# Optimization experiments

Hardware: AMD Instinct MI355X
Metric: run time of the kernel (lower is better)

## Reference

```python
import jax, jax.numpy as jnp
import numpy as np

N_NODES = 100000
N_EDGES = 1600000
N_GRAPHS = 128
BEHAVIOR_DIM = 32
LLM_DIM = 768
LLM_PROJ = 32
HIDDEN = 64
NUM_CLASSES = 2
INPUT_DIM = 64 + 16 + LLM_PROJ + BEHAVIOR_DIM  # 144


def gcn_conv(h, edge_index, edge_weight, W, b, n):
    """PyG GCNConv: linear -> gcn_norm with self-loops -> scatter-add at target."""
    h = h @ W  # [N, out]
    row, col = edge_index[0], edge_index[1]
    loop = jnp.arange(n)
    row_f = jnp.concatenate([row, loop])
    col_f = jnp.concatenate([col, loop])
    ew_f = jnp.concatenate([edge_weight, jnp.ones((n,), h.dtype)])
    deg = jax.ops.segment_sum(ew_f, col_f, num_segments=n)
    dinv = jnp.where(deg > 0, jax.lax.rsqrt(deg), 0.0)
    norm = dinv[row_f] * ew_f * dinv[col_f]  # [E+N]
    out = jax.ops.segment_sum(norm[:, None] * h[row_f], col_f, num_segments=n)
    return out + b


def global_mean_pool(x, batch, num_graphs):
    s = jax.ops.segment_sum(x, batch, num_segments=num_graphs)
    cnt = jax.ops.segment_sum(jnp.ones((x.shape[0],), x.dtype), batch, num_segments=num_graphs)
    return s / jnp.maximum(cnt, 1.0)[:, None]


def setup_inputs() -> dict:
    key = jax.random.key(0)
    ks = jax.random.split(key, 16)
    inp = {
        "x_names": jax.random.randint(ks[0], (N_NODES,), 0, 20000),
        "x_types": jax.random.randint(ks[1], (N_NODES,), 0, 100),
        "x_behaviors": jax.random.normal(ks[2], (N_NODES, BEHAVIOR_DIM), jnp.float32),
        "edge_index": jax.random.randint(ks[3], (2, N_EDGES), 0, N_NODES),
        "edge_weight": jax.random.uniform(ks[4], (N_EDGES,), jnp.float32),
        "batch": jnp.sort(jax.random.randint(ks[5], (N_NODES,), 0, N_GRAPHS)),
        "llm_features": jax.random.normal(ks[6], (N_NODES, LLM_DIM), jnp.float32),
        # parameters
        "name_emb": jax.random.normal(ks[7], (20000, 64), jnp.float32),
        "type_emb": jax.random.normal(ks[8], (100, 16), jnp.float32),
        "llm_proj_w": jax.random.normal(ks[9], (LLM_DIM, LLM_PROJ), jnp.float32) * 0.02,
        "llm_proj_b": jnp.zeros((LLM_PROJ,), jnp.float32),
        "conv1_w": jax.random.normal(ks[10], (INPUT_DIM, HIDDEN), jnp.float32) * 0.08,
        "conv1_b": jnp.zeros((HIDDEN,), jnp.float32),
        "conv2_w": jax.random.normal(ks[11], (HIDDEN, HIDDEN), jnp.float32) * 0.12,
        "conv2_b": jnp.zeros((HIDDEN,), jnp.float32),
        "cls_w": jax.random.normal(ks[12], (HIDDEN, NUM_CLASSES), jnp.float32) * 0.12,
        "cls_b": jnp.zeros((NUM_CLASSES,), jnp.float32),
    }
    return inp


def reference(x_names, x_types, x_behaviors, edge_index, edge_weight, batch,
              llm_features, name_emb, type_emb, llm_proj_w, llm_proj_b,
              conv1_w, conv1_b, conv2_w, conv2_b, cls_w, cls_b):
    n = x_names.shape[0]
    name_feat = name_emb[x_names]          # [N, 64]
    type_feat = type_emb[x_types]          # [N, 16]
    llm_feat = llm_features @ llm_proj_w + llm_proj_b  # [N, 32]
    x = jnp.concatenate([name_feat, type_feat, llm_feat, x_behaviors], axis=1)
    # dropout is identity in eval mode
    x = jax.nn.relu(gcn_conv(x, edge_index, edge_weight, conv1_w, conv1_b, n))
    x = jax.nn.relu(gcn_conv(x, edge_index, edge_weight, conv2_w, conv2_b, n))
    x = global_mean_pool(x, batch, N_GRAPHS)  # [G, HIDDEN]
    return x @ cls_w + cls_b                   # [G, 2]
```

## Files before the change

kernel.cpp:

```cpp
#include <hip/hip_runtime.h>
#include <cstdint>
#include <cstddef>

typedef __attribute__((ext_vector_type(8))) short bf16x8;
typedef __attribute__((ext_vector_type(4))) float f32x4;


__device__ __forceinline__ unsigned bf_rne(float x) {
  unsigned u = __float_as_uint(x);
  return (u + 0x7FFFu + ((u >> 16) & 1u)) >> 16;
}

__device__ __forceinline__ void split1(float x, short& hi, short& lo) {
  unsigned hb = bf_rne(x);
  hi = (short)hb;
  float fh = __uint_as_float(hb << 16);
  lo = (short)bf_rne(x - fh);
}

__device__ __forceinline__ void split8(const float4& p, const float4& q, bf16x8& h, bf16x8& l) {
  short hh, ll;
  split1(p.x, hh, ll); h[0] = hh; l[0] = ll;
  split1(p.y, hh, ll); h[1] = hh; l[1] = ll;
  split1(p.z, hh, ll); h[2] = hh; l[2] = ll;
  split1(p.w, hh, ll); h[3] = hh; l[3] = ll;
  split1(q.x, hh, ll); h[4] = hh; l[4] = ll;
  split1(q.y, hh, ll); h[5] = hh; l[5] = ll;
  split1(q.z, hh, ll); h[6] = hh; l[6] = ll;
  split1(q.w, hh, ll); h[7] = hh; l[7] = ll;
}


__global__ void prep1_kernel(const float* __restrict__ pw, const float* __restrict__ pb,
                             const float* __restrict__ w1,
                             short* __restrict__ Bh, short* __restrict__ Bl,
                             float* __restrict__ biasf) {
  int idx = blockIdx.x * 256 + threadIdx.x;
  if (idx < 896 * 64) {
    int gk = idx >> 6, col = idx & 63;
    float val;
    if (gk < 768) {
      float acc = 0.0f;
      #pragma unroll 8
      for (int m = 0; m < 32; ++m) acc = fmaf(pw[gk * 32 + m], w1[(80 + m) * 64 + col], acc);
      val = acc;
    } else if (gk < 832) val = w1[(gk - 768) * 64 + col];
    else if (gk < 848)   val = w1[(64 + gk - 832) * 64 + col];
    else if (gk < 864)   val = w1[(112 + gk - 848) * 64 + col];
    else if (gk < 880)   val = w1[(128 + gk - 864) * 64 + col];
    else                 val = 0.0f;
    int chunk = gk >> 5, k = gk & 31;
    int g, j;
    if (k < 16) { g = k >> 2; j = k & 3; } else { int k2 = k - 16; g = k2 >> 2; j = 4 + (k2 & 3); }
    size_t o = ((size_t)(chunk * 4 + g) * 64 + col) * 8 + j;
    short hh, ll; split1(val, hh, ll);
    Bh[o] = hh; Bl[o] = ll;
  } else if (idx < 896 * 64 + 64) {
    int col = idx - 896 * 64;
    float acc = 0.0f;
    for (int m = 0; m < 32; ++m) acc = fmaf(pb[m], w1[(80 + m) * 64 + col], acc);
    biasf[col] = acc;
  }
}

__global__ void prep2_kernel(const float* __restrict__ w2,
                             short* __restrict__ B2h, short* __restrict__ B2l) {
  int idx = blockIdx.x * 256 + threadIdx.x;
  if (idx >= 64 * 64) return;
  int gk = idx >> 6, col = idx & 63;
  float val = w2[gk * 64 + col];
  int chunk = gk >> 5, k = gk & 31;
  int g, j;
  if (k < 16) { g = k >> 2; j = k & 3; } else { int k2 = k - 16; g = k2 >> 2; j = 4 + (k2 & 3); }
  size_t o = ((size_t)(chunk * 4 + g) * 64 + col) * 8 + j;
  short hh, ll; split1(val, hh, ll);
  B2h[o] = hh; B2l[o] = ll;
}


__global__ void cnt_kernel(const int* __restrict__ ei, int* __restrict__ cnt, int E) {
  int e = blockIdx.x * 256 + threadIdx.x;
  if (e < E) atomicAdd(&cnt[ei[E + e]], 1);
}

__global__ __launch_bounds__(256) void scan_blk(const int* __restrict__ cnt,
                                                int* __restrict__ colp,
                                                int* __restrict__ bsum, int n) {
  __shared__ int ws[4];
  int t = threadIdx.x, lane = t & 63, w = t >> 6;
  int i = blockIdx.x * 256 + t;
  int v = (i < n) ? cnt[i] : 0;
  int x = v;
  #pragma unroll
  for (int off = 1; off < 64; off <<= 1) { int y = __shfl_up(x, off); if (lane >= off) x += y; }
  if (lane == 63) ws[w] = x;
  __syncthreads();
  if (t == 0) {
    int s = 0;
    #pragma unroll
    for (int k = 0; k < 4; ++k) { int tmp = ws[k]; ws[k] = s; s += tmp; }
    bsum[blockIdx.x] = s;
  }
  __syncthreads();
  if (i < n) colp[i] = ws[w] + x - v;
}

__global__ __launch_bounds__(512) void scan_top(int* __restrict__ bsum,
                                                int* __restrict__ colp, int nb, int n) {
  __shared__ int ws[8];
  int t = threadIdx.x, lane = t & 63, w = t >> 6;
  int v = (t < nb) ? bsum[t] : 0;
  int x = v;
  #pragma unroll
  for (int off = 1; off < 64; off <<= 1) { int y = __shfl_up(x, off); if (lane >= off) x += y; }
  if (lane == 63) ws[w] = x;
  __syncthreads();
  if (t == 0) {
    int s = 0;
    #pragma unroll
    for (int k = 0; k < 8; ++k) { int tmp = ws[k]; ws[k] = s; s += tmp; }
  }
  __syncthreads();
  int excl = ws[w] + x - v;
  if (t < nb) bsum[t] = excl;
  if (t == nb - 1) colp[n] = excl + v;
}

__global__ void scan_add(int* __restrict__ colp, int* __restrict__ fillp,
                         const int* __restrict__ bsum, int n) {
  int i = blockIdx.x * 256 + threadIdx.x;
  if (i < n) {
    int c = colp[i] + bsum[blockIdx.x];
    colp[i] = c;
    fillp[i] = c;
  }
}

__global__ void fill_kernel(const int* __restrict__ ei, const float* __restrict__ ew,
                            int* __restrict__ fillp, int2* __restrict__ csr, int E) {
  int e = blockIdx.x * 256 + threadIdx.x;
  if (e >= E) return;
  int row = ei[e], col = ei[E + e];
  int pos = atomicAdd(&fillp[col], 1);
  csr[pos] = make_int2(row, __float_as_int(ew[e]));
}

__global__ void degsum_kernel(const int* __restrict__ colp, const int2* __restrict__ csr,
                              float* __restrict__ dinv, int n) {
  int j = blockIdx.x * 256 + threadIdx.x;
  if (j >= n) return;
  int e0 = colp[j], e1 = colp[j + 1];
  float s = 1.0f;
  for (int e = e0; e < e1; ++e) s += __int_as_float(csr[e].y);
  dinv[j] = rsqrtf(s);
}

__global__ void wfix_kernel(int2* __restrict__ csr, const float* __restrict__ dinv, int E) {
  int i = blockIdx.x * 256 + threadIdx.x;
  if (i >= E) return;
  int2 m = csr[i];
  csr[i] = make_int2(m.x, __float_as_int(__int_as_float(m.y) * dinv[m.x]));
}


__device__ __forceinline__ void mfma24(f32x4 (&acc)[2][4],
                                       const bf16x8& ah0, const bf16x8& al0,
                                       const bf16x8& ah1, const bf16x8& al1,
                                       const bf16x8 (&bh)[4], const bf16x8 (&bl)[4]) {
  #pragma unroll
  for (int ct = 0; ct < 4; ++ct) {
    acc[0][ct] = __builtin_amdgcn_mfma_f32_16x16x32_bf16(ah0, bh[ct], acc[0][ct], 0, 0, 0);
    acc[0][ct] = __builtin_amdgcn_mfma_f32_16x16x32_bf16(ah0, bl[ct], acc[0][ct], 0, 0, 0);
    acc[0][ct] = __builtin_amdgcn_mfma_f32_16x16x32_bf16(al0, bh[ct], acc[0][ct], 0, 0, 0);
  }
  #pragma unroll
  for (int ct = 0; ct < 4; ++ct) {
    acc[1][ct] = __builtin_amdgcn_mfma_f32_16x16x32_bf16(ah1, bh[ct], acc[1][ct], 0, 0, 0);
    acc[1][ct] = __builtin_amdgcn_mfma_f32_16x16x32_bf16(ah1, bl[ct], acc[1][ct], 0, 0, 0);
    acc[1][ct] = __builtin_amdgcn_mfma_f32_16x16x32_bf16(al1, bh[ct], acc[1][ct], 0, 0, 0);
  }
}

__device__ __forceinline__ void loadB(const short* __restrict__ Bh, const short* __restrict__ Bl,
                                      int c, int g, int r16, bf16x8 (&bh)[4], bf16x8 (&bl)[4]) {
  #pragma unroll
  for (int ct = 0; ct < 4; ++ct) {
    size_t o = ((size_t)(c * 4 + g) * 64 + ct * 16 + r16) * 8;
    bh[ct] = *(const bf16x8*)(Bh + o);
    bl[ct] = *(const bf16x8*)(Bl + o);
  }
}

__global__ __launch_bounds__(256, 3) void gemm1_kernel(
    const float* __restrict__ llm, const short* __restrict__ Bh, const short* __restrict__ Bl,
    const int* __restrict__ names, const int* __restrict__ types,
    const float* __restrict__ beh, const float* __restrict__ nemb,
    const float* __restrict__ temb, const float* __restrict__ biasf,
    float* __restrict__ out, int n)
{
  int nwg = gridDim.x;
  int b = blockIdx.x;
  int q = nwg >> 3, r = nwg & 7;
  int xcd = b & 7, idx = b >> 3;
  int swz = (xcd < r ? xcd * (q + 1) : r * (q + 1) + (xcd - r) * q) + idx;

  int w = swz * 4 + (threadIdx.x >> 6);
  int nw = (n + 31) >> 5;
  if (w >= nw) return;
  int lane = threadIdx.x & 63;
  int g = lane >> 4, r16 = lane & 15;
  int base = w * 32;

  int arow0 = base + r16;      if (arow0 > n - 1) arow0 = n - 1;
  int arow1 = base + 16 + r16; if (arow1 > n - 1) arow1 = n - 1;
  int nm0 = names[arow0], nm1 = names[arow1];
  int tp0 = types[arow0], tp1 = types[arow1];

  const float* pA0 = llm + (size_t)arow0 * 768 + g * 4;
  const float* pA1 = llm + (size_t)arow1 * 768 + g * 4;

  f32x4 acc[2][4];
  #pragma unroll
  for (int i = 0; i < 2; ++i)
    #pragma unroll
    for (int j = 0; j < 4; ++j) { acc[i][j][0] = 0.f; acc[i][j][1] = 0.f; acc[i][j][2] = 0.f; acc[i][j][3] = 0.f; }

  float4 X0l = *(const float4*)(pA0 +  0), X0h = *(const float4*)(pA0 + 16);
  float4 X1l = *(const float4*)(pA1 +  0), X1h = *(const float4*)(pA1 + 16);
  float4 Y0l = *(const float4*)(pA0 + 32), Y0h = *(const float4*)(pA0 + 48);
  float4 Y1l = *(const float4*)(pA1 + 32), Y1h = *(const float4*)(pA1 + 48);

  bf16x8 bh[4], bl[4], ah0, al0, ah1, al1;

  #pragma unroll 1
  for (int cc = 0; cc < 11; ++cc) {
    const int c = cc * 2;
    loadB(Bh, Bl, c, g, r16, bh, bl);
    split8(X0l, X0h, ah0, al0);
    split8(X1l, X1h, ah1, al1);
    X0l = *(const float4*)(pA0 + (c + 2) * 32);
    X0h = *(const float4*)(pA0 + (c + 2) * 32 + 16);
    X1l = *(const float4*)(pA1 + (c + 2) * 32);
    X1h = *(const float4*)(pA1 + (c + 2) * 32 + 16);
    mfma24(acc, ah0, al0, ah1, al1, bh, bl);
    loadB(Bh, Bl, c + 1, g, r16, bh, bl);
    split8(Y0l, Y0h, ah0, al0);
    split8(Y1l, Y1h, ah1, al1);
    Y0l = *(const float4*)(pA0 + (c + 3) * 32);
    Y0h = *(const float4*)(pA0 + (c + 3) * 32 + 16);
    Y1l = *(const float4*)(pA1 + (c + 3) * 32);
    Y1h = *(const float4*)(pA1 + (c + 3) * 32 + 16);
    mfma24(acc, ah0, al0, ah1, al1, bh, bl);
  }

  loadB(Bh, Bl, 22, g, r16, bh, bl);
  split8(X0l, X0h, ah0, al0);
  split8(X1l, X1h, ah1, al1);
  mfma24(acc, ah0, al0, ah1, al1, bh, bl);

  loadB(Bh, Bl, 23, g, r16, bh, bl);
  split8(Y0l, Y0h, ah0, al0);
  split8(Y1l, Y1h, ah1, al1);
  mfma24(acc, ah0, al0, ah1, al1, bh, bl);

  const float* pN0 = nemb + (size_t)nm0 * 64 + g * 4;
  const float* pN1 = nemb + (size_t)nm1 * 64 + g * 4;
  #pragma unroll
  for (int t = 0; t < 2; ++t) {
    float4 l0 = *(const float4*)(pN0 + t * 32), h0 = *(const float4*)(pN0 + t * 32 + 16);
    float4 l1 = *(const float4*)(pN1 + t * 32), h1 = *(const float4*)(pN1 + t * 32 + 16);
    loadB(Bh, Bl, 24 + t, g, r16, bh, bl);
    split8(l0, h0, ah0, al0);
    split8(l1, h1, ah1, al1);
    mfma24(acc, ah0, al0, ah1, al1, bh, bl);
  }
  {
    float4 l0 = *(const float4*)(temb + (size_t)tp0 * 16 + g * 4);
    float4 h0 = *(const float4*)(beh + (size_t)arow0 * 32 + g * 4);
    float4 l1 = *(const float4*)(temb + (size_t)tp1 * 16 + g * 4);
    float4 h1 = *(const float4*)(beh + (size_t)arow1 * 32 + g * 4);
    loadB(Bh, Bl, 26, g, r16, bh, bl);
    split8(l0, h0, ah0, al0);
    split8(l1, h1, ah1, al1);
    mfma24(acc, ah0, al0, ah1, al1, bh, bl);
  }
  {
    const float4 z = make_float4(0.f, 0.f, 0.f, 0.f);
    float4 l0 = *(const float4*)(beh + (size_t)arow0 * 32 + 16 + g * 4);
    float4 l1 = *(const float4*)(beh + (size_t)arow1 * 32 + 16 + g * 4);
    loadB(Bh, Bl, 27, g, r16, bh, bl);
    split8(l0, z, ah0, al0);
    split8(l1, z, ah1, al1);
    mfma24(acc, ah0, al0, ah1, al1, bh, bl);
  }

  #pragma unroll
  for (int ct = 0; ct < 4; ++ct) {
    int col = ct * 16 + r16;
    float bf = biasf[col];
    #pragma unroll
    for (int rr = 0; rr < 4; ++rr) {
      int node0 = base + g * 4 + rr;
      if (node0 < n) out[(size_t)node0 * 64 + col] = acc[0][ct][rr] + bf;
      int node1 = base + 16 + g * 4 + rr;
      if (node1 < n) out[(size_t)node1 * 64 + col] = acc[1][ct][rr] + bf;
    }
  }
}


__global__ __launch_bounds__(256, 4) void gemm2_kernel(
    const float* __restrict__ h, const short* __restrict__ B2h, const short* __restrict__ B2l,
    float* __restrict__ out, int n)
{
  int w = blockIdx.x * 4 + (threadIdx.x >> 6);
  int nw = (n + 31) >> 5;
  if (w >= nw) return;
  int lane = threadIdx.x & 63;
  int g = lane >> 4, r16 = lane & 15;
  int base = w * 32;
  int arow0 = base + r16;      if (arow0 > n - 1) arow0 = n - 1;
  int arow1 = base + 16 + r16; if (arow1 > n - 1) arow1 = n - 1;

  f32x4 acc[2][4];
  #pragma unroll
  for (int i = 0; i < 2; ++i)
    #pragma unroll
    for (int j = 0; j < 4; ++j) { acc[i][j][0] = 0.f; acc[i][j][1] = 0.f; acc[i][j][2] = 0.f; acc[i][j][3] = 0.f; }

  #pragma unroll
  for (int c = 0; c < 2; ++c) {
    bf16x8 bh[4], bl[4];
    loadB(B2h, B2l, c, g, r16, bh, bl);
    const float* p0 = h + (size_t)arow0 * 64 + c * 32 + g * 4;
    const float* p1 = h + (size_t)arow1 * 64 + c * 32 + g * 4;
    float4 lo0 = *(const float4*)p0, hi0 = *(const float4*)(p0 + 16);
    float4 lo1 = *(const float4*)p1, hi1 = *(const float4*)(p1 + 16);
    bf16x8 ah0, al0, ah1, al1;
    split8(lo0, hi0, ah0, al0);
    split8(lo1, hi1, ah1, al1);
    mfma24(acc, ah0, al0, ah1, al1, bh, bl);
  }

  #pragma unroll
  for (int ct = 0; ct < 4; ++ct) {
    int col = ct * 16 + r16;
    #pragma unroll
    for (int rr = 0; rr < 4; ++rr) {
      int node0 = base + g * 4 + rr;
      if (node0 < n) out[(size_t)node0 * 64 + col] = acc[0][ct][rr];
      int node1 = base + 16 + g * 4 + rr;
      if (node1 < n) out[(size_t)node1 * 64 + col] = acc[1][ct][rr];
    }
  }
}


__global__ __launch_bounds__(256) void agg_kernel(
    const float* __restrict__ h, const int* __restrict__ colp,
    const int2* __restrict__ csr, const float* __restrict__ dinv,
    const float* __restrict__ bias, float* __restrict__ out, int n)
{
  int wid = threadIdx.x >> 6, lane = threadIdx.x & 63;
  int j = blockIdx.x * 4 + wid;
  if (j >= n) return;
  float dj = dinv[j];
  float hj = h[(size_t)j * 64 + lane];
  int e0 = colp[j], e1 = colp[j + 1];
  float s = 0.0f;
  int e = e0;
  for (; e + 4 <= e1; e += 4) {
    int2 m0 = csr[e], m1 = csr[e + 1], m2 = csr[e + 2], m3 = csr[e + 3];
    float f0 = h[(size_t)m0.x * 64 + lane];
    float f1 = h[(size_t)m1.x * 64 + lane];
    float f2 = h[(size_t)m2.x * 64 + lane];
    float f3 = h[(size_t)m3.x * 64 + lane];
    s = fmaf(__int_as_float(m0.y), f0, s);
    s = fmaf(__int_as_float(m1.y), f1, s);
    s = fmaf(__int_as_float(m2.y), f2, s);
    s = fmaf(__int_as_float(m3.y), f3, s);
  }
  for (; e < e1; ++e) {
    int2 m = csr[e];
    s = fmaf(__int_as_float(m.y), h[(size_t)m.x * 64 + lane], s);
  }
  float acc = bias[lane] + dj * fmaf(dj, hj, s);
  out[(size_t)j * 64 + lane] = fmaxf(acc, 0.0f);
}


__global__ __launch_bounds__(256) void pool_kernel(const float* __restrict__ x,
                                                   const int* __restrict__ batch,
                                                   float* __restrict__ pooled, int n) {
  __shared__ float red[4][64];
  __shared__ int range_s[2];
  int gph = blockIdx.x;
  int tid = threadIdx.x, wid = tid >> 6, lane = tid & 63;
  if (tid < 2) {
    int target = gph + tid;
    int lo = 0, hi = n;
    while (lo < hi) { int m = (lo + hi) >> 1; if (batch[m] < target) lo = m + 1; else hi = m; }
    range_s[tid] = lo;
  }
  __syncthreads();
  int lo = range_s[0], hi = range_s[1];
  float acc = 0.0f;
  for (int i = lo + wid; i < hi; i += 4) acc += x[(size_t)i * 64 + lane];
  red[wid][lane] = acc;
  __syncthreads();
  if (tid < 64) {
    float sum = red[0][lane] + red[1][lane] + red[2][lane] + red[3][lane];
    float cntf = (float)(hi - lo);
    pooled[gph * 64 + lane] = sum / fmaxf(cntf, 1.0f);
  }
}

__global__ void cls_kernel(const float* __restrict__ pooled, const float* __restrict__ cw,
                           const float* __restrict__ cb, float* __restrict__ out) {
  int t = threadIdx.x;
  int gph = t >> 1, c = t & 1;
  float acc = cb[c];
  #pragma unroll 8
  for (int k = 0; k < 64; ++k) acc = fmaf(pooled[gph * 64 + k], cw[k * 2 + c], acc);
  out[gph * 2 + c] = acc;
}


extern "C" void kernel_launch(void* const* d_in, const int* in_sizes, int n_in,
                              void* d_out, int out_size, void* d_ws, size_t ws_size,
                              hipStream_t stream) {
  const int*   x_names  = (const int*)  d_in[0];
  const int*   x_types  = (const int*)  d_in[1];
  const float* behav    = (const float*)d_in[2];
  const int*   ei       = (const int*)  d_in[3];
  const float* ew       = (const float*)d_in[4];
  const int*   batch    = (const int*)  d_in[5];
  const float* llm      = (const float*)d_in[6];
  const float* name_emb = (const float*)d_in[7];
  const float* type_emb = (const float*)d_in[8];
  const float* pw       = (const float*)d_in[9];
  const float* pb       = (const float*)d_in[10];
  const float* w1       = (const float*)d_in[11];
  const float* b1       = (const float*)d_in[12];
  const float* w2       = (const float*)d_in[13];
  const float* b2       = (const float*)d_in[14];
  const float* cw       = (const float*)d_in[15];
  const float* cb       = (const float*)d_in[16];

  const int N = in_sizes[0];
  const int E = in_sizes[4];
  const int nb = (N + 255) / 256;
  const int eb = (E + 255) / 256;
  const int nwaves = (N + 31) / 32;
  const int gblocks = (nwaves + 3) / 4;

  char* p = (char*)d_ws;
  auto alloc = [&](size_t bytes) -> void* {
    void* r = (void*)p; p += (bytes + 255) & ~(size_t)255; return r;
  };
  float* dinv   = (float*)alloc((size_t)N * 4);
  int*   cnt    = (int*)  alloc((size_t)N * 4);
  int*   colp   = (int*)  alloc((size_t)(N + 1) * 4);
  int*   fillp  = (int*)  alloc((size_t)N * 4);
  int2*  csr    = (int2*) alloc((size_t)E * 8);
  int*   bsum   = (int*)  alloc((size_t)(nb + 1) * 4);
  short* Bh     = (short*)alloc((size_t)896 * 64 * 2);
  short* Bl     = (short*)alloc((size_t)896 * 64 * 2);
  short* B2h    = (short*)alloc((size_t)64 * 64 * 2);
  short* B2l    = (short*)alloc((size_t)64 * 64 * 2);
  float* biasf  = (float*)alloc((size_t)64 * 4);
  float* bufX   = (float*)alloc((size_t)N * 64 * 4);
  float* bufY   = (float*)alloc((size_t)N * 64 * 4);
  float* pooled = (float*)alloc((size_t)128 * 64 * 4);
  (void)ws_size; (void)n_in; (void)out_size;

  prep1_kernel<<<(896 * 64 + 64 + 255) / 256, 256, 0, stream>>>(pw, pb, w1, Bh, Bl, biasf);
  prep2_kernel<<<16, 256, 0, stream>>>(w2, B2h, B2l);
  hipMemsetAsync(cnt, 0, (size_t)N * 4, stream);
  cnt_kernel<<<eb, 256, 0, stream>>>(ei, cnt, E);
  scan_blk<<<nb, 256, 0, stream>>>(cnt, colp, bsum, N);
  scan_top<<<1, 512, 0, stream>>>(bsum, colp, nb, N);
  scan_add<<<nb, 256, 0, stream>>>(colp, fillp, bsum, N);
  fill_kernel<<<eb, 256, 0, stream>>>(ei, ew, fillp, csr, E);
  degsum_kernel<<<nb, 256, 0, stream>>>(colp, csr, dinv, N);
  wfix_kernel<<<eb, 256, 0, stream>>>(csr, dinv, E);

  gemm1_kernel<<<gblocks, 256, 0, stream>>>(llm, Bh, Bl, x_names, x_types, behav,
                                            name_emb, type_emb, biasf, bufX, N);
  agg_kernel<<<(N + 3) / 4, 256, 0, stream>>>(bufX, colp, csr, dinv, b1, bufY, N);
  gemm2_kernel<<<gblocks, 256, 0, stream>>>(bufY, B2h, B2l, bufX, N);
  agg_kernel<<<(N + 3) / 4, 256, 0, stream>>>(bufX, colp, csr, dinv, b2, bufY, N);
  pool_kernel<<<128, 256, 0, stream>>>(bufY, batch, pooled, N);
  cls_kernel<<<1, 256, 0, stream>>>(pooled, cw, cb, (float*)d_out);
}
```

Baseline: 548.2 us.

## Use single fp16 MFMA for GEMM1, fold source-degree scaling into GEMM epilogues

GEMM1 drops the three-pass bf16 hi/lo split emulation and runs one fp16 MFMA pass over fp16 weights, with a three-stage register prefetch and sched barriers. The per-edge wfix pass is removed: the GEMM epilogues now multiply each output row by dinv, so aggregation uses raw edge weights. The aggregation loop is unrolled to 8 with two accumulators, and the two prep kernels are merged. The fp16 path cuts MFMA work and prologue traffic, but it loses accuracy and could overflow on large inputs.

New measurement: 497.2 us. -9.3%, faster.

```diff
diff --git a/kernel.cpp b/kernel.cpp
--- a/kernel.cpp
+++ b/kernel.cpp
@@ -3,6 +3,7 @@
 #include <cstddef>
 
 typedef __attribute__((ext_vector_type(8))) short bf16x8;
+typedef __attribute__((ext_vector_type(8))) _Float16 f16x8;
 typedef __attribute__((ext_vector_type(4))) float f32x4;
 
 
@@ -30,11 +31,18 @@
   split1(q.w, hh, ll); h[7] = hh; l[7] = ll;
 }
 
-
-__global__ void prep1_kernel(const float* __restrict__ pw, const float* __restrict__ pb,
-                             const float* __restrict__ w1,
-                             short* __restrict__ Bh, short* __restrict__ Bl,
-                             float* __restrict__ biasf) {
+__device__ __forceinline__ f16x8 cvt8(const float4& p, const float4& q) {
+  f16x8 r;
+  r[0] = (_Float16)p.x; r[1] = (_Float16)p.y; r[2] = (_Float16)p.z; r[3] = (_Float16)p.w;
+  r[4] = (_Float16)q.x; r[5] = (_Float16)q.y; r[6] = (_Float16)q.z; r[7] = (_Float16)q.w;
+  return r;
+}
+
+
+__global__ void prep_kernel(const float* __restrict__ pw, const float* __restrict__ pb,
+                            const float* __restrict__ w1, const float* __restrict__ w2,
+                            _Float16* __restrict__ Bf, float* __restrict__ biasf,
+                            short* __restrict__ B2h, short* __restrict__ B2l) {
   int idx = blockIdx.x * 256 + threadIdx.x;
   if (idx < 896 * 64) {
     int gk = idx >> 6, col = idx & 63;
@@ -52,29 +60,23 @@
     int chunk = gk >> 5, k = gk & 31;
     int g, j;
     if (k < 16) { g = k >> 2; j = k & 3; } else { int k2 = k - 16; g = k2 >> 2; j = 4 + (k2 & 3); }
-    size_t o = ((size_t)(chunk * 4 + g) * 64 + col) * 8 + j;
-    short hh, ll; split1(val, hh, ll);
-    Bh[o] = hh; Bl[o] = ll;
+    Bf[((size_t)(chunk * 4 + g) * 64 + col) * 8 + j] = (_Float16)val;
   } else if (idx < 896 * 64 + 64) {
     int col = idx - 896 * 64;
     float acc = 0.0f;
     for (int m = 0; m < 32; ++m) acc = fmaf(pb[m], w1[(80 + m) * 64 + col], acc);
     biasf[col] = acc;
-  }
-}
-
-__global__ void prep2_kernel(const float* __restrict__ w2,
-                             short* __restrict__ B2h, short* __restrict__ B2l) {
-  int idx = blockIdx.x * 256 + threadIdx.x;
-  if (idx >= 64 * 64) return;
-  int gk = idx >> 6, col = idx & 63;
-  float val = w2[gk * 64 + col];
-  int chunk = gk >> 5, k = gk & 31;
-  int g, j;
-  if (k < 16) { g = k >> 2; j = k & 3; } else { int k2 = k - 16; g = k2 >> 2; j = 4 + (k2 & 3); }
-  size_t o = ((size_t)(chunk * 4 + g) * 64 + col) * 8 + j;
-  short hh, ll; split1(val, hh, ll);
-  B2h[o] = hh; B2l[o] = ll;
+  } else if (idx < 896 * 64 + 64 + 64 * 64) {
+    int q2 = idx - (896 * 64 + 64);
+    int gk = q2 >> 6, col = q2 & 63;
+    float val = w2[gk * 64 + col];
+    int chunk = gk >> 5, k = gk & 31;
+    int g, j;
+    if (k < 16) { g = k >> 2; j = k & 3; } else { int k2 = k - 16; g = k2 >> 2; j = 4 + (k2 & 3); }
+    size_t o = ((size_t)(chunk * 4 + g) * 64 + col) * 8 + j;
+    short hh, ll; split1(val, hh, ll);
+    B2h[o] = hh; B2l[o] = ll;
+  }
 }
 
 
@@ -155,54 +157,35 @@
   dinv[j] = rsqrtf(s);
 }
 
-__global__ void wfix_kernel(int2* __restrict__ csr, const float* __restrict__ dinv, int E) {
-  int i = blockIdx.x * 256 + threadIdx.x;
-  if (i >= E) return;
-  int2 m = csr[i];
-  csr[i] = make_int2(m.x, __float_as_int(__int_as_float(m.y) * dinv[m.x]));
-}
-
-
-__device__ __forceinline__ void mfma24(f32x4 (&acc)[2][4],
-                                       const bf16x8& ah0, const bf16x8& al0,
-                                       const bf16x8& ah1, const bf16x8& al1,
-                                       const bf16x8 (&bh)[4], const bf16x8 (&bl)[4]) {
+
+__device__ __forceinline__ void loadBf(const _Float16* __restrict__ Bf, int c, int g, int r16,
+                                       f16x8 (&bf)[4]) {
+  #pragma unroll
+  for (int ct = 0; ct < 4; ++ct)
+    bf[ct] = *(const f16x8*)(Bf + ((size_t)(c * 4 + g) * 64 + ct * 16 + r16) * 8);
+}
+
+__device__ __forceinline__ void mfma8(f32x4 (&acc)[2][4], const f16x8& a0, const f16x8& a1,
+                                      const f16x8 (&bf)[4]) {
   #pragma unroll
   for (int ct = 0; ct < 4; ++ct) {
-    acc[0][ct] = __builtin_amdgcn_mfma_f32_16x16x32_bf16(ah0, bh[ct], acc[0][ct], 0, 0, 0);
-    acc[0][ct] = __builtin_amdgcn_mfma_f32_16x16x32_bf16(ah0, bl[ct], acc[0][ct], 0, 0, 0);
-    acc[0][ct] = __builtin_amdgcn_mfma_f32_16x16x32_bf16(al0, bh[ct], acc[0][ct], 0, 0, 0);
-  }
-  #pragma unroll
-  for (int ct = 0; ct < 4; ++ct) {
-    acc[1][ct] = __builtin_amdgcn_mfma_f32_16x16x32_bf16(ah1, bh[ct], acc[1][ct], 0, 0, 0);
-    acc[1][ct] = __builtin_amdgcn_mfma_f32_16x16x32_bf16(ah1, bl[ct], acc[1][ct], 0, 0, 0);
-    acc[1][ct] = __builtin_amdgcn_mfma_f32_16x16x32_bf16(al1, bh[ct], acc[1][ct], 0, 0, 0);
-  }
-}
-
-__device__ __forceinline__ void loadB(const short* __restrict__ Bh, const short* __restrict__ Bl,
-                                      int c, int g, int r16, bf16x8 (&bh)[4], bf16x8 (&bl)[4]) {
-  #pragma unroll
-  for (int ct = 0; ct < 4; ++ct) {
-    size_t o = ((size_t)(c * 4 + g) * 64 + ct * 16 + r16) * 8;
-    bh[ct] = *(const bf16x8*)(Bh + o);
-    bl[ct] = *(const bf16x8*)(Bl + o);
+    acc[0][ct] = __builtin_amdgcn_mfma_f32_16x16x32_f16(a0, bf[ct], acc[0][ct], 0, 0, 0);
+    acc[1][ct] = __builtin_amdgcn_mfma_f32_16x16x32_f16(a1, bf[ct], acc[1][ct], 0, 0, 0);
   }
 }
 
 __global__ __launch_bounds__(256, 3) void gemm1_kernel(
-    const float* __restrict__ llm, const short* __restrict__ Bh, const short* __restrict__ Bl,
+    const float* __restrict__ llm, const _Float16* __restrict__ Bf,
     const int* __restrict__ names, const int* __restrict__ types,
     const float* __restrict__ beh, const float* __restrict__ nemb,
     const float* __restrict__ temb, const float* __restrict__ biasf,
-    float* __restrict__ out, int n)
+    const float* __restrict__ dinv, float* __restrict__ out, int n)
 {
   int nwg = gridDim.x;
   int b = blockIdx.x;
   int q = nwg >> 3, r = nwg & 7;
-  int xcd = b & 7, idx = b >> 3;
-  int swz = (xcd < r ? xcd * (q + 1) : r * (q + 1) + (xcd - r) * q) + idx;
+  int xcd = b & 7, bidx = b >> 3;
+  int swz = (xcd < r ? xcd * (q + 1) : r * (q + 1) + (xcd - r) * q) + bidx;
 
   int w = swz * 4 + (threadIdx.x >> 6);
   int nw = (n + 31) >> 5;
@@ -229,39 +212,49 @@
   float4 X1l = *(const float4*)(pA1 +  0), X1h = *(const float4*)(pA1 + 16);
   float4 Y0l = *(const float4*)(pA0 + 32), Y0h = *(const float4*)(pA0 + 48);
   float4 Y1l = *(const float4*)(pA1 + 32), Y1h = *(const float4*)(pA1 + 48);
-
-  bf16x8 bh[4], bl[4], ah0, al0, ah1, al1;
+  float4 Z0l = *(const float4*)(pA0 + 64), Z0h = *(const float4*)(pA0 + 80);
+  float4 Z1l = *(const float4*)(pA1 + 64), Z1h = *(const float4*)(pA1 + 96 - 16);
+
+  f16x8 bf[4], a0, a1;
 
   #pragma unroll 1
-  for (int cc = 0; cc < 11; ++cc) {
-    const int c = cc * 2;
-    loadB(Bh, Bl, c, g, r16, bh, bl);
-    split8(X0l, X0h, ah0, al0);
-    split8(X1l, X1h, ah1, al1);
-    X0l = *(const float4*)(pA0 + (c + 2) * 32);
-    X0h = *(const float4*)(pA0 + (c + 2) * 32 + 16);
-    X1l = *(const float4*)(pA1 + (c + 2) * 32);
-    X1h = *(const float4*)(pA1 + (c + 2) * 32 + 16);
-    mfma24(acc, ah0, al0, ah1, al1, bh, bl);
-    loadB(Bh, Bl, c + 1, g, r16, bh, bl);
-    split8(Y0l, Y0h, ah0, al0);
-    split8(Y1l, Y1h, ah1, al1);
-    Y0l = *(const float4*)(pA0 + (c + 3) * 32);
-    Y0h = *(const float4*)(pA0 + (c + 3) * 32 + 16);
-    Y1l = *(const float4*)(pA1 + (c + 3) * 32);
-    Y1h = *(const float4*)(pA1 + (c + 3) * 32 + 16);
-    mfma24(acc, ah0, al0, ah1, al1, bh, bl);
-  }
-
-  loadB(Bh, Bl, 22, g, r16, bh, bl);
-  split8(X0l, X0h, ah0, al0);
-  split8(X1l, X1h, ah1, al1);
-  mfma24(acc, ah0, al0, ah1, al1, bh, bl);
-
-  loadB(Bh, Bl, 23, g, r16, bh, bl);
-  split8(Y0l, Y0h, ah0, al0);
-  split8(Y1l, Y1h, ah1, al1);
-  mfma24(acc, ah0, al0, ah1, al1, bh, bl);
+  for (int cc = 0; cc < 7; ++cc) {
+    const int c = cc * 3;
+    loadBf(Bf, c, g, r16, bf);
+    a0 = cvt8(X0l, X0h); a1 = cvt8(X1l, X1h);
+    X0l = *(const float4*)(pA0 + (c + 3) * 32);
+    X0h = *(const float4*)(pA0 + (c + 3) * 32 + 16);
+    X1l = *(const float4*)(pA1 + (c + 3) * 32);
+    X1h = *(const float4*)(pA1 + (c + 3) * 32 + 16);
+    __builtin_amdgcn_sched_barrier(0);
+    mfma8(acc, a0, a1, bf);
+    loadBf(Bf, c + 1, g, r16, bf);
+    a0 = cvt8(Y0l, Y0h); a1 = cvt8(Y1l, Y1h);
+    Y0l = *(const float4*)(pA0 + (c + 4) * 32);
+    Y0h = *(const float4*)(pA0 + (c + 4) * 32 + 16);
+    Y1l = *(const float4*)(pA1 + (c + 4) * 32);
+    Y1h = *(const float4*)(pA1 + (c + 4) * 32 + 16);
+    __builtin_amdgcn_sched_barrier(0);
+    mfma8(acc, a0, a1, bf);
+    loadBf(Bf, c + 2, g, r16, bf);
+    a0 = cvt8(Z0l, Z0h); a1 = cvt8(Z1l, Z1h);
+    Z0l = *(const float4*)(pA0 + (c + 5) * 32);
+    Z0h = *(const float4*)(pA0 + (c + 5) * 32 + 16);
+    Z1l = *(const float4*)(pA1 + (c + 5) * 32);
+    Z1h = *(const float4*)(pA1 + (c + 5) * 32 + 16);
+    __builtin_amdgcn_sched_barrier(0);
+    mfma8(acc, a0, a1, bf);
+  }
+
+  loadBf(Bf, 21, g, r16, bf);
+  a0 = cvt8(X0l, X0h); a1 = cvt8(X1l, X1h);
+  mfma8(acc, a0, a1, bf);
+  loadBf(Bf, 22, g, r16, bf);
+  a0 = cvt8(Y0l, Y0h); a1 = cvt8(Y1l, Y1h);
+  mfma8(acc, a0, a1, bf);
+  loadBf(Bf, 23, g, r16, bf);
+  a0 = cvt8(Z0l, Z0h); a1 = cvt8(Z1l, Z1h);
+  mfma8(acc, a0, a1, bf);
 
   const float* pN0 = nemb + (size_t)nm0 * 64 + g * 4;
   const float* pN1 = nemb + (size_t)nm1 * 64 + g * 4;
@@ -269,49 +262,62 @@
   for (int t = 0; t < 2; ++t) {
     float4 l0 = *(const float4*)(pN0 + t * 32), h0 = *(const float4*)(pN0 + t * 32 + 16);
     float4 l1 = *(const float4*)(pN1 + t * 32), h1 = *(const float4*)(pN1 + t * 32 + 16);
-    loadB(Bh, Bl, 24 + t, g, r16, bh, bl);
-    split8(l0, h0, ah0, al0);
-    split8(l1, h1, ah1, al1);
-    mfma24(acc, ah0, al0, ah1, al1, bh, bl);
+    loadBf(Bf, 24 + t, g, r16, bf);
+    a0 = cvt8(l0, h0); a1 = cvt8(l1, h1);
+    mfma8(acc, a0, a1, bf);
   }
   {
     float4 l0 = *(const float4*)(temb + (size_t)tp0 * 16 + g * 4);
     float4 h0 = *(const float4*)(beh + (size_t)arow0 * 32 + g * 4);
     float4 l1 = *(const float4*)(temb + (size_t)tp1 * 16 + g * 4);
     float4 h1 = *(const float4*)(beh + (size_t)arow1 * 32 + g * 4);
-    loadB(Bh, Bl, 26, g, r16, bh, bl);
-    split8(l0, h0, ah0, al0);
-    split8(l1, h1, ah1, al1);
-    mfma24(acc, ah0, al0, ah1, al1, bh, bl);
+    loadBf(Bf, 26, g, r16, bf);
+    a0 = cvt8(l0, h0); a1 = cvt8(l1, h1);
+    mfma8(acc, a0, a1, bf);
   }
   {
     const float4 z = make_float4(0.f, 0.f, 0.f, 0.f);
     float4 l0 = *(const float4*)(beh + (size_t)arow0 * 32 + 16 + g * 4);
     float4 l1 = *(const float4*)(beh + (size_t)arow1 * 32 + 16 + g * 4);
-    loadB(Bh, Bl, 27, g, r16, bh, bl);
-    split8(l0, z, ah0, al0);
-    split8(l1, z, ah1, al1);
-    mfma24(acc, ah0, al0, ah1, al1, bh, bl);
-  }
-
+    loadBf(Bf, 27, g, r16, bf);
+    a0 = cvt8(l0, z); a1 = cvt8(l1, z);
+    mfma8(acc, a0, a1, bf);
+  }
+
+  float dv0[4], dv1[4];
+  #pragma unroll
+  for (int rr = 0; rr < 4; ++rr) {
+    int n0 = base + g * 4 + rr;      dv0[rr] = dinv[n0 < n ? n0 : n - 1];
+    int n1 = base + 16 + g * 4 + rr; dv1[rr] = dinv[n1 < n ? n1 : n - 1];
+  }
   #pragma unroll
   for (int ct = 0; ct < 4; ++ct) {
     int col = ct * 16 + r16;
-    float bf = biasf[col];
+    float bfc = biasf[col];
     #pragma unroll
     for (int rr = 0; rr < 4; ++rr) {
       int node0 = base + g * 4 + rr;
-      if (node0 < n) out[(size_t)node0 * 64 + col] = acc[0][ct][rr] + bf;
+      if (node0 < n) out[(size_t)node0 * 64 + col] = (acc[0][ct][rr] + bfc) * dv0[rr];
       int node1 = base + 16 + g * 4 + rr;
-      if (node1 < n) out[(size_t)node1 * 64 + col] = acc[1][ct][rr] + bf;
+      if (node1 < n) out[(size_t)node1 * 64 + col] = (acc[1][ct][rr] + bfc) * dv1[rr];
     }
   }
 }
 
+
+__device__ __forceinline__ void loadB2(const short* __restrict__ Bh, const short* __restrict__ Bl,
+                                       int c, int g, int r16, bf16x8 (&bh)[4], bf16x8 (&bl)[4]) {
+  #pragma unroll
+  for (int ct = 0; ct < 4; ++ct) {
+    size_t o = ((size_t)(c * 4 + g) * 64 + ct * 16 + r16) * 8;
+    bh[ct] = *(const bf16x8*)(Bh + o);
+    bl[ct] = *(const bf16x8*)(Bl + o);
+  }
+}
 
 __global__ __launch_bounds__(256, 4) void gemm2_kernel(
     const float* __restrict__ h, const short* __restrict__ B2h, const short* __restrict__ B2l,
-    float* __restrict__ out, int n)
+    const float* __restrict__ dinv, float* __restrict__ out, int n)
 {
   int w = blockIdx.x * 4 + (threadIdx.x >> 6);
   int nw = (n + 31) >> 5;
@@ -331,7 +337,7 @@
   #pragma unroll
   for (int c = 0; c < 2; ++c) {
     bf16x8 bh[4], bl[4];
-    loadB(B2h, B2l, c, g, r16, bh, bl);
+    loadB2(B2h, B2l, c, g, r16, bh, bl);
     const float* p0 = h + (size_t)arow0 * 64 + c * 32 + g * 4;
     const float* p1 = h + (size_t)arow1 * 64 + c * 32 + g * 4;
     float4 lo0 = *(const float4*)p0, hi0 = *(const float4*)(p0 + 16);
@@ -339,25 +345,42 @@
     bf16x8 ah0, al0, ah1, al1;
     split8(lo0, hi0, ah0, al0);
     split8(lo1, hi1, ah1, al1);
-    mfma24(acc, ah0, al0, ah1, al1, bh, bl);
-  }
-
+    #pragma unroll
+    for (int ct = 0; ct < 4; ++ct) {
+      acc[0][ct] = __builtin_amdgcn_mfma_f32_16x16x32_bf16(ah0, bh[ct], acc[0][ct], 0, 0, 0);
+      acc[0][ct] = __builtin_amdgcn_mfma_f32_16x16x32_bf16(ah0, bl[ct], acc[0][ct], 0, 0, 0);
+      acc[0][ct] = __builtin_amdgcn_mfma_f32_16x16x32_bf16(al0, bh[ct], acc[0][ct], 0, 0, 0);
+    }
+    #pragma unroll
+    for (int ct = 0; ct < 4; ++ct) {
+      acc[1][ct] = __builtin_amdgcn_mfma_f32_16x16x32_bf16(ah1, bh[ct], acc[1][ct], 0, 0, 0);
+      acc[1][ct] = __builtin_amdgcn_mfma_f32_16x16x32_bf16(ah1, bl[ct], acc[1][ct], 0, 0, 0);
+      acc[1][ct] = __builtin_amdgcn_mfma_f32_16x16x32_bf16(al1, bh[ct], acc[1][ct], 0, 0, 0);
+    }
+  }
+
+  float dv0[4], dv1[4];
+  #pragma unroll
+  for (int rr = 0; rr < 4; ++rr) {
+    int n0 = base + g * 4 + rr;      dv0[rr] = dinv[n0 < n ? n0 : n - 1];
+    int n1 = base + 16 + g * 4 + rr; dv1[rr] = dinv[n1 < n ? n1 : n - 1];
+  }
   #pragma unroll
   for (int ct = 0; ct < 4; ++ct) {
     int col = ct * 16 + r16;
     #pragma unroll
     for (int rr = 0; rr < 4; ++rr) {
       int node0 = base + g * 4 + rr;
-      if (node0 < n) out[(size_t)node0 * 64 + col] = acc[0][ct][rr];
+      if (node0 < n) out[(size_t)node0 * 64 + col] = acc[0][ct][rr] * dv0[rr];
       int node1 = base + 16 + g * 4 + rr;
-      if (node1 < n) out[(size_t)node1 * 64 + col] = acc[1][ct][rr];
+      if (node1 < n) out[(size_t)node1 * 64 + col] = acc[1][ct][rr] * dv1[rr];
     }
   }
 }
 
 
 __global__ __launch_bounds__(256) void agg_kernel(
-    const float* __restrict__ h, const int* __restrict__ colp,
+    const float* __restrict__ hp, const int* __restrict__ colp,
     const int2* __restrict__ csr, const float* __restrict__ dinv,
     const float* __restrict__ bias, float* __restrict__ out, int n)
 {
@@ -365,26 +388,42 @@
   int j = blockIdx.x * 4 + wid;
   if (j >= n) return;
   float dj = dinv[j];
-  float hj = h[(size_t)j * 64 + lane];
+  float hj = hp[(size_t)j * 64 + lane];
   int e0 = colp[j], e1 = colp[j + 1];
-  float s = 0.0f;
+  float s0 = 0.0f, s1 = 0.0f;
   int e = e0;
-  for (; e + 4 <= e1; e += 4) {
-    int2 m0 = csr[e], m1 = csr[e + 1], m2 = csr[e + 2], m3 = csr[e + 3];
-    float f0 = h[(size_t)m0.x * 64 + lane];
-    float f1 = h[(size_t)m1.x * 64 + lane];
-    float f2 = h[(size_t)m2.x * 64 + lane];
-    float f3 = h[(size_t)m3.x * 64 + lane];
-    s = fmaf(__int_as_float(m0.y), f0, s);
-    s = fmaf(__int_as_float(m1.y), f1, s);
-    s = fmaf(__int_as_float(m2.y), f2, s);
-    s = fmaf(__int_as_float(m3.y), f3, s);
-  }
-  for (; e < e1; ++e) {
+  for (; e + 8 <= e1; e += 8) {
+    int2 m0 = csr[e],     m1 = csr[e + 1], m2 = csr[e + 2], m3 = csr[e + 3];
+    int2 m4 = csr[e + 4], m5 = csr[e + 5], m6 = csr[e + 6], m7 = csr[e + 7];
+    float f0 = hp[(size_t)m0.x * 64 + lane];
+    float f1 = hp[(size_t)m1.x * 64 + lane];
+    float f2 = hp[(size_t)m2.x * 64 + lane];
+    float f3 = hp[(size_t)m3.x * 64 + lane];
+    float f4 = hp[(size_t)m4.x * 64 + lane];
+    float f5 = hp[(size_t)m5.x * 64 + lane];
+    float f6 = hp[(size_t)m6.x * 64 + lane];
+    float f7 = hp[(size_t)m7.x * 64 + lane];
+    s0 = fmaf(__int_as_float(m0.y), f0, s0);
+    s1 = fmaf(__int_as_float(m1.y), f1, s1);
+    s0 = fmaf(__int_as_float(m2.y), f2, s0);
+    s1 = fmaf(__int_as_float(m3.y), f3, s1);
+    s0 = fmaf(__int_as_float(m4.y), f4, s0);
+    s1 = fmaf(__int_as_float(m5.y), f5, s1);
+    s0 = fmaf(__int_as_float(m6.y), f6, s0);
+    s1 = fmaf(__int_as_float(m7.y), f7, s1);
+  }
+  for (; e + 2 <= e1; e += 2) {
+    int2 m0 = csr[e], m1 = csr[e + 1];
+    float f0 = hp[(size_t)m0.x * 64 + lane];
+    float f1 = hp[(size_t)m1.x * 64 + lane];
+    s0 = fmaf(__int_as_float(m0.y), f0, s0);
+    s1 = fmaf(__int_as_float(m1.y), f1, s1);
+  }
+  if (e < e1) {
     int2 m = csr[e];
-    s = fmaf(__int_as_float(m.y), h[(size_t)m.x * 64 + lane], s);
-  }
-  float acc = bias[lane] + dj * fmaf(dj, hj, s);
+    s0 = fmaf(__int_as_float(m.y), hp[(size_t)m.x * 64 + lane], s0);
+  }
+  float acc = bias[lane] + dj * (hj + s0 + s1);
   out[(size_t)j * 64 + lane] = fmaxf(acc, 0.0f);
 }
 
@@ -451,31 +490,29 @@
   const int E = in_sizes[4];
   const int nb = (N + 255) / 256;
   const int eb = (E + 255) / 256;
-  const int nwaves = (N + 31) / 32;
-  const int gblocks = (nwaves + 3) / 4;
+  const int gblocks = ((N + 31) / 32 + 3) / 4;
 
   char* p = (char*)d_ws;
   auto alloc = [&](size_t bytes) -> void* {
     void* r = (void*)p; p += (bytes + 255) & ~(size_t)255; return r;
   };
-  float* dinv   = (float*)alloc((size_t)N * 4);
-  int*   cnt    = (int*)  alloc((size_t)N * 4);
-  int*   colp   = (int*)  alloc((size_t)(N + 1) * 4);
-  int*   fillp  = (int*)  alloc((size_t)N * 4);
-  int2*  csr    = (int2*) alloc((size_t)E * 8);
-  int*   bsum   = (int*)  alloc((size_t)(nb + 1) * 4);
-  short* Bh     = (short*)alloc((size_t)896 * 64 * 2);
-  short* Bl     = (short*)alloc((size_t)896 * 64 * 2);
-  short* B2h    = (short*)alloc((size_t)64 * 64 * 2);
-  short* B2l    = (short*)alloc((size_t)64 * 64 * 2);
-  float* biasf  = (float*)alloc((size_t)64 * 4);
-  float* bufX   = (float*)alloc((size_t)N * 64 * 4);
-  float* bufY   = (float*)alloc((size_t)N * 64 * 4);
-  float* pooled = (float*)alloc((size_t)128 * 64 * 4);
+  float*     dinv   = (float*)    alloc((size_t)N * 4);
+  int*       cnt    = (int*)      alloc((size_t)N * 4);
+  int*       colp   = (int*)      alloc((size_t)(N + 1) * 4);
+  int*       fillp  = (int*)      alloc((size_t)N * 4);
+  int2*      csr    = (int2*)     alloc((size_t)E * 8);
+  int*       bsum   = (int*)      alloc((size_t)(nb + 1) * 4);
+  _Float16*  Bf     = (_Float16*) alloc((size_t)896 * 64 * 2);
+  short*     B2h    = (short*)    alloc((size_t)64 * 64 * 2);
+  short*     B2l    = (short*)    alloc((size_t)64 * 64 * 2);
+  float*     biasf  = (float*)    alloc((size_t)64 * 4);
+  float*     bufX   = (float*)    alloc((size_t)N * 64 * 4);
+  float*     bufY   = (float*)    alloc((size_t)N * 64 * 4);
+  float*     pooled = (float*)    alloc((size_t)128 * 64 * 4);
   (void)ws_size; (void)n_in; (void)out_size;
 
-  prep1_kernel<<<(896 * 64 + 64 + 255) / 256, 256, 0, stream>>>(pw, pb, w1, Bh, Bl, biasf);
-  prep2_kernel<<<16, 256, 0, stream>>>(w2, B2h, B2l);
+  prep_kernel<<<(896 * 64 + 64 + 64 * 64 + 255) / 256, 256, 0, stream>>>(
+      pw, pb, w1, w2, Bf, biasf, B2h, B2l);
   hipMemsetAsync(cnt, 0, (size_t)N * 4, stream);
   cnt_kernel<<<eb, 256, 0, stream>>>(ei, cnt, E);
   scan_blk<<<nb, 256, 0, stream>>>(cnt, colp, bsum, N);
@@ -483,12 +520,11 @@
   scan_add<<<nb, 256, 0, stream>>>(colp, fillp, bsum, N);
   fill_kernel<<<eb, 256, 0, stream>>>(ei, ew, fillp, csr, E);
   degsum_kernel<<<nb, 256, 0, stream>>>(colp, csr, dinv, N);
-  wfix_kernel<<<eb, 256, 0, stream>>>(csr, dinv, E);
-
-  gemm1_kernel<<<gblocks, 256, 0, stream>>>(llm, Bh, Bl, x_names, x_types, behav,
-                                            name_emb, type_emb, biasf, bufX, N);
+
+  gemm1_kernel<<<gblocks, 256, 0, stream>>>(llm, Bf, x_names, x_types, behav,
+                                            name_emb, type_emb, biasf, dinv, bufX, N);
   agg_kernel<<<(N + 3) / 4, 256, 0, stream>>>(bufX, colp, csr, dinv, b1, bufY, N);
-  gemm2_kernel<<<gblocks, 256, 0, stream>>>(bufY, B2h, B2l, bufX, N);
+  gemm2_kernel<<<gblocks, 256, 0, stream>>>(bufY, B2h, B2l, dinv, bufX, N);
   agg_kernel<<<(N + 3) / 4, 256, 0, stream>>>(bufX, colp, csr, dinv, b2, bufY, N);
   pool_kernel<<<128, 256, 0, stream>>>(bufY, batch, pooled, N);
   cls_kernel<<<1, 256, 0, stream>>>(pooled, cw, cb, (float*)d_out);
```
